# Kernel tuning notes

Hardware: AMD Instinct MI355X
Metric: run time of the kernel (lower is better)

The kernel has to match this reference:

```python
import jax, jax.numpy as jnp
import numpy as np

B, C, D, H, W = 4, 1, 192, 192, 192
SMALL = 4            # int(192 * bias_scale=0.025)
BIAS_STD = 0.7
MAX_SIGMA = 3.0
TRUNCATE = 4.0
K = 2 * int(TRUNCATE * MAX_SIGMA) + 1   # fixed truncated kernel size = 25
N_LABELS = 32
TABLE = 128          # static remap-table size (>= max source label, >= max dest)


def setup_inputs() -> dict:
    key = jax.random.key(0)
    k1, k2, k3, k4, k5 = jax.random.split(key, 5)
    return {
        "x": jax.random.normal(k1, (B, C, D, H, W), jnp.float32),
        "small_bias": jax.random.normal(k2, (B, 1, SMALL, SMALL, SMALL), jnp.float32),
        "sigma01": jax.random.uniform(k3, (B, 3), jnp.float32),
        "labels": jax.random.randint(k4, (B, 1, D, H, W), 0, N_LABELS, jnp.int32),
        "source_values": jnp.arange(N_LABELS, dtype=jnp.int64),
        "dest_values": jax.random.randint(k5, (N_LABELS,), 0, 100, jnp.int64),
    }


def _lin_weights(n_in, n_out):
    """Dense 1D linear-interp matrix [n_out, n_in], align_corners=True."""
    pos = jnp.linspace(0.0, n_in - 1.0, n_out)
    i0 = jnp.clip(jnp.floor(pos).astype(jnp.int32), 0, n_in - 2)
    f = pos - i0.astype(pos.dtype)
    r = jnp.arange(n_out)
    Wm = jnp.zeros((n_out, n_in), jnp.float32)
    Wm = Wm.at[r, i0].add(1.0 - f).at[r, i0 + 1].add(f)
    return Wm


def _bias_field(small_bias):
    # trilinear align_corners upsample [B,1,s,s,s] -> [B,1,D,H,W], separable
    b = small_bias * BIAS_STD
    b = jnp.einsum('bcxyz,dx->bcdyz', b, _lin_weights(SMALL, D))
    b = jnp.einsum('bcdyz,hy->bcdhz', b, _lin_weights(SMALL, H))
    b = jnp.einsum('bcdhz,wz->bcdhw', b, _lin_weights(SMALL, W))
    return b


def _gauss_kernels(sigma):
    """sigma [3] -> normalized kernels [3, K]; identity (delta) where sigma<0.01."""
    ar = jnp.arange(K, dtype=jnp.float32) - K // 2
    s = jnp.maximum(sigma, 1e-3)[:, None]
    g = jnp.exp(-0.5 * (ar[None, :] ** 2) / (s ** 2))
    g = g / g.sum(-1, keepdims=True)
    delta = jnp.zeros((K,), jnp.float32).at[K // 2].set(1.0)
    return jnp.where(sigma[:, None] >= 0.01, g, delta[None, :])


def _blur_axis(x, k, axis):
    # x [C,D,H,W]; depthwise 1D conv along `axis` with replicate (edge) padding
    p = K // 2
    xm = jnp.moveaxis(x, axis, -1)
    shp = xm.shape
    xm = xm.reshape(-1, 1, shp[-1])
    xm = jnp.pad(xm, ((0, 0), (0, 0), (p, p)), mode='edge')
    out = jax.lax.conv_general_dilated(xm, k.reshape(1, 1, K), (1,), 'VALID')
    return jnp.moveaxis(out.reshape(shp), -1, axis)


def _blur_sample(x, kernels):
    # x [C,D,H,W], kernels [3,K]; separable blur over D,H,W
    for i, ax in enumerate((1, 2, 3)):
        x = _blur_axis(x, kernels[i], ax)
    return x


def reference(x, small_bias, sigma01, labels, source_values, dest_values):
    # 1) bias-field corruption: x * exp(upsampled random field)
    img = x * jnp.exp(_bias_field(small_bias))
    # 2) dynamic per-sample Gaussian blur, sigma in [0, MAX_SIGMA]
    kernels = jax.vmap(_gauss_kernels)(sigma01 * MAX_SIGMA)   # [B,3,K]
    img = jax.vmap(_blur_sample)(img, kernels)
    # 3) label remap via lookup table gather
    mapping = jnp.zeros((TABLE,), jnp.int32).at[source_values].set(
        dest_values.astype(jnp.int32))
    labels_out = mapping[labels]
    return img, labels_out
```

## Files before the change

### kernel.cpp

```cpp
#include <hip/hip_runtime.h>
#include <hip/hip_fp16.h>
#include <cstdint>
#include <cstddef>

#define Bc 4
#define Dd 192
#define Hh 192
#define Ww 192
#define KK 25
#define RR 12
#define VOL (Bc*Dd*Hh*Ww)
#define SP 216
#define SPU (SP/2)
#define SH 98
#define RIN 56
#define RD  56

typedef unsigned short u16;
typedef unsigned int   u32;
typedef __fp16 h2 __attribute__((ext_vector_type(2)));
typedef __fp16 h8 __attribute__((ext_vector_type(8)));
typedef float  f32x4 __attribute__((ext_vector_type(4)));

__device__ inline u32 pk2(float a, float b) {
    return __builtin_bit_cast(u32, __builtin_amdgcn_cvt_pkrtz(a, b));
}

__global__ void setup_tables_kernel(const float* __restrict__ sigma01,
                                    const int* __restrict__ src,
                                    const int* __restrict__ dst,
                                    u32* __restrict__ kern2,
                                    int* __restrict__ mapping,
                                    float* __restrict__ mapf) {
    int t = threadIdx.x;
    if (t < 128) mapping[t] = 0;
    __syncthreads();
    if (t < 32) {
        int s = src[t];
        if (s >= 0 && s < 128) mapping[s] = dst[t];
    }
    __syncthreads();
    if (t < 128) mapf[t] = (float)mapping[t];
    if (t < Bc * 3) {
        float sig = sigma01[t] * 3.0f;
        float s = fmaxf(sig, 1e-3f);
        float g[KK];
        float sum = 0.0f;
        #pragma unroll
        for (int i = 0; i < KK; i++) {
            float a = (float)(i - RR);
            float v = expf(-0.5f * a * a / (s * s));
            g[i] = v; sum += v;
        }
        float inv = 1.0f / sum;
        #pragma unroll
        for (int i = 0; i < KK; i++) {
            float v = g[i] * inv;
            if (sig < 0.01f) v = (i == RR) ? 1.0f : 0.0f;
            u16 hb = __builtin_bit_cast(u16, __float2half(v));
            kern2[t * KK + i] = (u32)hb | ((u32)hb << 16);
        }
    }
}

__global__ __launch_bounds__(256) void pass_wh_remap_kernel(
    const float* __restrict__ x, u16* __restrict__ outB,
    const u32* __restrict__ kern2, const float* __restrict__ sb,
    const int4* __restrict__ labels, float4* __restrict__ lab_out,
    const float* __restrict__ mapf) {
    __shared__ u16 P[RIN * SP];
    __shared__ float2 ch2[RIN * 3];
    __shared__ u16 kpadW[64];
    const int tid = threadIdx.x;
    const int hx = blockIdx.x;
    const int d  = blockIdx.y;
    const int b  = blockIdx.z;

    if (tid < RIN) {
        int r = tid;
        int hrow = min(max(32 * hx - RR + r, 0), Hh - 1);
        float pos_d = d * (3.0f / 191.0f);
        int   id0   = min((int)pos_d, 2);
        float fd    = pos_d - (float)id0;
        float pos_h = hrow * (3.0f / 191.0f);
        int   ih0   = min((int)pos_h, 2);
        float fh    = pos_h - (float)ih0;
        const float* sbA = sb + b * 64 + id0 * 16 + ih0 * 4;
        float c[4];
        #pragma unroll
        for (int k = 0; k < 4; k++) {
            float v00 = sbA[k],      v01 = sbA[4 + k];
            float v10 = sbA[16 + k], v11 = sbA[20 + k];
            float vd0 = (1.f - fd) * v00 + fd * v10;
            float vd1 = (1.f - fd) * v01 + fd * v11;
            c[k] = ((1.f - fh) * vd0 + fh * vd1) * 0.7f;
        }
        #pragma unroll
        for (int k = 0; k < 3; k++)
            ch2[r * 3 + k] = make_float2(c[k], c[k + 1] - c[k]);
    }
    if (tid >= 64 && tid < 128) {
        int i = tid - 64;
        int t = i - 15;
        u16 v = (t >= 0 && t < KK) ? (u16)(kern2[(b * 3 + 2) * KK + t] & 0xFFFFu)
                                   : (u16)0;
        kpadW[i] = v;
    }
    __syncthreads();

    const size_t pbase = ((size_t)b * Dd + d) * (size_t)(Hh * Ww);
    #pragma unroll
    for (int it = 0; it < 11; it++) {
        int i4 = it * 256 + tid;
        if (i4 < RIN * 48) {
            int r = i4 / 48, w4 = i4 % 48;
            int w = 4 * w4;
            int hrow = min(max(32 * hx - RR + r, 0), Hh - 1);
            float4 v = *(const float4*)(x + pbase + (size_t)hrow * Ww + w);
            float rs[4];
            #pragma unroll
            for (int j = 0; j < 4; j++) {
                float pw = (float)(w + j) * (3.0f / 191.0f);
                int sel = (pw >= 1.0f) + (pw >= 2.0f);
                float2 cd = ch2[r * 3 + sel];
                float bias = fmaf(pw - (float)sel, cd.y, cd.x);
                float val = (j == 0 ? v.x : j == 1 ? v.y : j == 2 ? v.z : v.w);
                rs[j] = val * __expf(bias);
            }
            u32* dstp = (u32*)&P[r * SP + RR + w];
            dstp[0] = pk2(rs[0], rs[1]);
            dstp[1] = pk2(rs[2], rs[3]);
            if (w4 == 0) {
                u32 hh = pk2(rs[0], rs[0]);
                u32* hp = (u32*)&P[r * SP];
                #pragma unroll
                for (int m = 0; m < 6; m++) hp[m] = hh;
            } else if (w4 == 47) {
                u32 hh = pk2(rs[3], rs[3]);
                u32* hp = (u32*)&P[r * SP + RR + Ww];
                #pragma unroll
                for (int m = 0; m < 6; m++) hp[m] = hh;
            }
        }
    }
    __syncthreads();

    {
        const int bid = (b * Dd + d) * 6 + hx;
        const int4* lp = labels + (size_t)bid * 1536 + tid;
        int4 lab[6];
        #pragma unroll
        for (int m = 0; m < 6; m++) lab[m] = lp[m * 256];
        float4* op = lab_out + (size_t)bid * 1536 + tid;
        #pragma unroll
        for (int m = 0; m < 6; m++) {
            int4 l = lab[m];
            float4 o;
            o.x = mapf[min(max(l.x, 0), 127)];
            o.y = mapf[min(max(l.y, 0), 127)];
            o.z = mapf[min(max(l.z, 0), 127)];
            o.w = mapf[min(max(l.w, 0), 127)];
            op[m * 256] = o;
        }
    }

    {
        const int ln = tid & 63, wv = tid >> 6;
        const int c  = ln & 15;
        const int kg = ln >> 4;
        h8 B0, B1;
        #pragma unroll
        for (int j = 0; j < 8; j++) {
            int k = kg * 8 + j;
            B0[j] = __builtin_bit_cast(__fp16, kpadW[15 + k - c]);
            int i1 = 15 + k + 32 - c;
            B1[j] = __builtin_bit_cast(__fp16, (i1 < 64) ? kpadW[i1] : (u16)0);
        }
        const int ra = min(wv * 16 + c, RIN - 1);
        const u16* rowp = &P[ra * SP + kg * 8];
        const int rd0 = wv * 16 + kg * 4;
        h8 F[10];
        #pragma unroll
        for (int f = 0; f < 10; f++)
            F[f] = __builtin_bit_cast(h8, *(const uint4*)(rowp + f * 16));
        #pragma unroll
        for (int ct = 0; ct < 8; ct++) {
            f32x4 acc = {0.f, 0.f, 0.f, 0.f};
            acc = __builtin_amdgcn_mfma_f32_16x16x32_f16(F[ct], B0, acc, 0, 0, 0);
            acc = __builtin_amdgcn_mfma_f32_16x16x32_f16(F[ct + 2], B1, acc, 0, 0, 0);
            #pragma unroll
            for (int m = 0; m < 4; m++) {
                int rd = rd0 + m;
                if (rd < RIN)
                    P[rd * SP + RR + ct * 16 + c] =
                        __builtin_bit_cast(u16, (__fp16)acc[m]);
            }
        }
        h8 G[4];
        G[0] = __builtin_bit_cast(h8, *(const uint4*)(rowp + 160));
        G[1] = __builtin_bit_cast(h8, *(const uint4*)(rowp + 176));
        G[2] = __builtin_bit_cast(h8, *(const uint4*)(rowp + ((kg == 0) ? 192 : 160)));
        G[3] = __builtin_bit_cast(h8, *(const uint4*)(rowp + ((kg == 0) ? 208 : 160)));
        #pragma unroll
        for (int ct = 8; ct < 12; ct++) {
            h8 A0 = (ct < 10) ? F[ct] : G[ct - 10];
            h8 A1 = G[ct - 8];
            f32x4 acc = {0.f, 0.f, 0.f, 0.f};
            acc = __builtin_amdgcn_mfma_f32_16x16x32_f16(A0, B0, acc, 0, 0, 0);
            acc = __builtin_amdgcn_mfma_f32_16x16x32_f16(A1, B1, acc, 0, 0, 0);
            #pragma unroll
            for (int m = 0; m < 4; m++) {
                int rd = rd0 + m;
                if (rd < RIN)
                    P[rd * SP + RR + ct * 16 + c] =
                        __builtin_bit_cast(u16, (__fp16)acc[m]);
            }
        }
    }
    __syncthreads();

    {
        const u32* kh2 = kern2 + (b * 3 + 1) * KK;
        u32* outp = (u32*)(outB + pbase);
        #pragma unroll
        for (int it = 0; it < 2; it++) {
            int item = it * 256 + tid;
            if (item < 384) {
                int col = item % 96;
                int g = item / 96;
                u32 win[32];
                #pragma unroll
                for (int i = 0; i < 32; i++)
                    win[i] = *((const u32*)P + (g * 8 + i) * SPU + 6 + col);
                h2 acc[8];
                #pragma unroll
                for (int j = 0; j < 8; j++) acc[j] = (h2)(0.0f);
                #pragma unroll
                for (int t = 0; t < KK; t++) {
                    h2 kv = __builtin_bit_cast(h2, kh2[t]);
                    #pragma unroll
                    for (int j = 0; j < 8; j++)
                        acc[j] += kv * __builtin_bit_cast(h2, win[j + t]);
                }
                #pragma unroll
                for (int j = 0; j < 8; j++)
                    outp[(32 * hx + g * 8 + j) * 96 + col] =
                        __builtin_bit_cast(u32, acc[j]);
            }
        }
    }
}

__global__ __launch_bounds__(192) void pass_d_kernel(
    const u16* __restrict__ in, float* __restrict__ img,
    const u32* __restrict__ kern2) {
    __shared__ __attribute__((aligned(16))) u16 T[RD * SH];
    const int tid = threadIdx.x;
    const int w0 = blockIdx.x * 96;
    const int d0 = blockIdx.y * 32;
    const int z = blockIdx.z;
    const int h = z % Hh, b = z / Hh;
    const u32* kp = kern2 + b * 3 * KK;
    #pragma unroll
    for (int k = 0; k < 4; k++) {
        int idx = k * 192 + tid;
        if (idx < RD * 12) {
            int r = idx / 12, sg = idx % 12;
            int dd = min(max(d0 + r - RR, 0), Dd - 1);
            uint4 v = *(const uint4*)(in + (((size_t)b * Dd + dd) * Hh + h) * (size_t)Ww + w0 + sg * 8);
            u32* p = (u32*)&T[r * SH + sg * 8];
            p[0] = v.x; p[1] = v.y; p[2] = v.z; p[3] = v.w;
        }
    }
    __syncthreads();
    const int p = tid % 48;
    const int g = tid / 48;
    const int ob = g * 8;
    u32 win[32];
    #pragma unroll
    for (int i = 0; i < 32; i++) win[i] = *(const u32*)&T[(ob + i) * SH + 2 * p];
    h2 acc[8];
    #pragma unroll
    for (int j = 0; j < 8; j++) acc[j] = (h2)(0.0f);
    #pragma unroll
    for (int t = 0; t < KK; t++) {
        h2 kv = __builtin_bit_cast(h2, kp[t]);
        #pragma unroll
        for (int j = 0; j < 8; j++)
            acc[j] += kv * __builtin_bit_cast(h2, win[j + t]);
    }
    #pragma unroll
    for (int j = 0; j < 8; j++) {
        h2 a = acc[j];
        float2 f = make_float2((float)a.x, (float)a.y);
        *(float2*)(img + (((size_t)b * Dd + (d0 + ob + j)) * Hh + h) * (size_t)Ww + w0 + 2 * p) = f;
    }
}

extern "C" void kernel_launch(void* const* d_in, const int* in_sizes, int n_in,
                              void* d_out, int out_size, void* d_ws, size_t ws_size,
                              hipStream_t stream) {
    const float* x          = (const float*)d_in[0];
    const float* small_bias = (const float*)d_in[1];
    const float* sigma01    = (const float*)d_in[2];
    const int*   labels     = (const int*)d_in[3];
    const int*   src        = (const int*)d_in[4];
    const int*   dst        = (const int*)d_in[5];

    float* out     = (float*)d_out;
    float* img     = out;
    float* lab_out = out + (size_t)VOL;

    u32*   kern2   = (u32*)((float*)d_ws + 384);
    int*   mapping = (int*)((float*)d_ws + 768);
    float* mapf    = (float*)d_ws + 896;
    u16*   Bb      = (u16*)((char*)d_ws + 8192);

    setup_tables_kernel<<<1, 128, 0, stream>>>(sigma01, src, dst, kern2,
                                               mapping, mapf);

    pass_wh_remap_kernel<<<dim3(6, Dd, Bc), 256, 0, stream>>>(
        x, Bb, kern2, small_bias,
        (const int4*)labels, (float4*)lab_out, mapf);
    pass_d_kernel<<<dim3(Ww / 96, Dd / 32, Bc * Hh), 192, 0, stream>>>(Bb, img, kern2);
}
```

Baseline: 134.3 us.

## Fold setup kernel into blur kernels by computing taps and remap table per block

Drops the separate setup_tables launch. Each block now computes its own Gaussian taps in-kernel with fast exp, and the W/H kernel builds the label remap table in shared memory. The point is to remove one kernel launch and its serialization, and to keep blur taps in registers instead of reading them from global memory. The W/H load loop is also changed so each thread handles a fixed column with its interpolation coefficients precomputed, using 240 active threads over 12 iterations. The cost is redundant tap math in every block, slightly different exp precision, and some idle threads in the load loop.

```diff
diff --git a/kernel.cpp b/kernel.cpp
--- a/kernel.cpp
+++ b/kernel.cpp
@@ -26,51 +26,32 @@
     return __builtin_bit_cast(u32, __builtin_amdgcn_cvt_pkrtz(a, b));
 }
 
-__global__ void setup_tables_kernel(const float* __restrict__ sigma01,
-                                    const int* __restrict__ src,
-                                    const int* __restrict__ dst,
-                                    u32* __restrict__ kern2,
-                                    int* __restrict__ mapping,
-                                    float* __restrict__ mapf) {
-    int t = threadIdx.x;
-    if (t < 128) mapping[t] = 0;
-    __syncthreads();
-    if (t < 32) {
-        int s = src[t];
-        if (s >= 0 && s < 128) mapping[s] = dst[t];
-    }
-    __syncthreads();
-    if (t < 128) mapf[t] = (float)mapping[t];
-    if (t < Bc * 3) {
-        float sig = sigma01[t] * 3.0f;
-        float s = fmaxf(sig, 1e-3f);
-        float g[KK];
-        float sum = 0.0f;
-        #pragma unroll
-        for (int i = 0; i < KK; i++) {
-            float a = (float)(i - RR);
-            float v = expf(-0.5f * a * a / (s * s));
-            g[i] = v; sum += v;
-        }
-        float inv = 1.0f / sum;
-        #pragma unroll
-        for (int i = 0; i < KK; i++) {
-            float v = g[i] * inv;
-            if (sig < 0.01f) v = (i == RR) ? 1.0f : 0.0f;
-            u16 hb = __builtin_bit_cast(u16, __float2half(v));
-            kern2[t * KK + i] = (u32)hb | ((u32)hb << 16);
-        }
-    }
+__device__ inline float gauss_tap(float s01, int idx) {
+    float sig = s01 * 3.0f;
+    float s = fmaxf(sig, 1e-3f);
+    float inv2 = -0.5f / (s * s);
+    float sum = 0.0f;
+    #pragma unroll
+    for (int i = 0; i < KK; i++) {
+        float a = (float)(i - RR);
+        sum += __expf(a * a * inv2);
+    }
+    float a = (float)(idx - RR);
+    float v = __expf(a * a * inv2) / sum;
+    if (sig < 0.01f) v = (idx == RR) ? 1.0f : 0.0f;
+    return v;
 }
 
 __global__ __launch_bounds__(256) void pass_wh_remap_kernel(
     const float* __restrict__ x, u16* __restrict__ outB,
-    const u32* __restrict__ kern2, const float* __restrict__ sb,
-    const int4* __restrict__ labels, float4* __restrict__ lab_out,
-    const float* __restrict__ mapf) {
+    const float* __restrict__ sigma01, const float* __restrict__ sb,
+    const int* __restrict__ src, const int* __restrict__ dst,
+    const int4* __restrict__ labels, float4* __restrict__ lab_out) {
     __shared__ u16 P[RIN * SP];
     __shared__ float2 ch2[RIN * 3];
     __shared__ u16 kpadW[64];
+    __shared__ u32 khp[25];
+    __shared__ float Lmap[128];
     const int tid = threadIdx.x;
     const int hx = blockIdx.x;
     const int d  = blockIdx.y;
@@ -99,47 +80,70 @@
         for (int k = 0; k < 3; k++)
             ch2[r * 3 + k] = make_float2(c[k], c[k + 1] - c[k]);
     }
-    if (tid >= 64 && tid < 128) {
-        int i = tid - 64;
-        int t = i - 15;
-        u16 v = (t >= 0 && t < KK) ? (u16)(kern2[(b * 3 + 2) * KK + t] & 0xFFFFu)
-                                   : (u16)0;
+    if (tid >= 56 && tid < 184) Lmap[tid - 56] = 0.0f;
+    if (tid >= 56 && tid < 81) {
+        int i = tid - 56;
+        float v = gauss_tap(sigma01[b * 3 + 1], i);
+        u16 hb = __builtin_bit_cast(u16, __float2half(v));
+        khp[i] = (u32)hb | ((u32)hb << 16);
+    }
+    if (tid >= 184 && tid < 248) {
+        int i = tid - 184;
+        int tt = i - 15;
+        u16 v = 0;
+        if (tt >= 0 && tt < KK)
+            v = __builtin_bit_cast(u16, __float2half(gauss_tap(sigma01[b * 3 + 2], tt)));
         kpadW[i] = v;
     }
     __syncthreads();
 
+    if (tid < 32) {
+        int s = src[tid];
+        if (s >= 0 && s < 128) Lmap[s] = (float)dst[tid];
+    }
+
     const size_t pbase = ((size_t)b * Dd + d) * (size_t)(Hh * Ww);
-    #pragma unroll
-    for (int it = 0; it < 11; it++) {
-        int i4 = it * 256 + tid;
-        if (i4 < RIN * 48) {
-            int r = i4 / 48, w4 = i4 % 48;
-            int w = 4 * w4;
-            int hrow = min(max(32 * hx - RR + r, 0), Hh - 1);
-            float4 v = *(const float4*)(x + pbase + (size_t)hrow * Ww + w);
-            float rs[4];
-            #pragma unroll
-            for (int j = 0; j < 4; j++) {
-                float pw = (float)(w + j) * (3.0f / 191.0f);
-                int sel = (pw >= 1.0f) + (pw >= 2.0f);
-                float2 cd = ch2[r * 3 + sel];
-                float bias = fmaf(pw - (float)sel, cd.y, cd.x);
-                float val = (j == 0 ? v.x : j == 1 ? v.y : j == 2 ? v.z : v.w);
-                rs[j] = val * __expf(bias);
-            }
-            u32* dstp = (u32*)&P[r * SP + RR + w];
-            dstp[0] = pk2(rs[0], rs[1]);
-            dstp[1] = pk2(rs[2], rs[3]);
-            if (w4 == 0) {
-                u32 hh = pk2(rs[0], rs[0]);
-                u32* hp = (u32*)&P[r * SP];
-                #pragma unroll
-                for (int m = 0; m < 6; m++) hp[m] = hh;
-            } else if (w4 == 47) {
-                u32 hh = pk2(rs[3], rs[3]);
-                u32* hp = (u32*)&P[r * SP + RR + Ww];
-                #pragma unroll
-                for (int m = 0; m < 6; m++) hp[m] = hh;
+    {
+        const int w4 = tid % 48;
+        const int rloc = tid / 48;
+        const int w = 4 * w4;
+        float fwj[4];
+        int   selj[4];
+        #pragma unroll
+        for (int j = 0; j < 4; j++) {
+            float pw = (float)(w + j) * (3.0f / 191.0f);
+            int sel = (pw >= 1.0f) + (pw >= 2.0f);
+            selj[j] = sel;
+            fwj[j] = pw - (float)sel;
+        }
+        #pragma unroll
+        for (int it = 0; it < 12; it++) {
+            int row = it * 5 + rloc;
+            if (tid < 240 && row < RIN) {
+                int hrow = min(max(32 * hx - RR + row, 0), Hh - 1);
+                float4 v = *(const float4*)(x + pbase + (size_t)hrow * Ww + w);
+                float rs[4];
+                #pragma unroll
+                for (int j = 0; j < 4; j++) {
+                    float2 cd = ch2[row * 3 + selj[j]];
+                    float bias = fmaf(fwj[j], cd.y, cd.x);
+                    float val = (j == 0 ? v.x : j == 1 ? v.y : j == 2 ? v.z : v.w);
+                    rs[j] = val * __expf(bias);
+                }
+                u32* dstp = (u32*)&P[row * SP + RR + w];
+                dstp[0] = pk2(rs[0], rs[1]);
+                dstp[1] = pk2(rs[2], rs[3]);
+                if (w4 == 0) {
+                    u32 hh = pk2(rs[0], rs[0]);
+                    u32* hp = (u32*)&P[row * SP];
+                    #pragma unroll
+                    for (int m = 0; m < 6; m++) hp[m] = hh;
+                } else if (w4 == 47) {
+                    u32 hh = pk2(rs[3], rs[3]);
+                    u32* hp = (u32*)&P[row * SP + RR + Ww];
+                    #pragma unroll
+                    for (int m = 0; m < 6; m++) hp[m] = hh;
+                }
             }
         }
     }
@@ -156,10 +160,10 @@
         for (int m = 0; m < 6; m++) {
             int4 l = lab[m];
             float4 o;
-            o.x = mapf[min(max(l.x, 0), 127)];
-            o.y = mapf[min(max(l.y, 0), 127)];
-            o.z = mapf[min(max(l.z, 0), 127)];
-            o.w = mapf[min(max(l.w, 0), 127)];
+            o.x = Lmap[min(max(l.x, 0), 127)];
+            o.y = Lmap[min(max(l.y, 0), 127)];
+            o.z = Lmap[min(max(l.z, 0), 127)];
+            o.w = Lmap[min(max(l.w, 0), 127)];
             op[m * 256] = o;
         }
     }
@@ -220,7 +224,9 @@
     __syncthreads();
 
     {
-        const u32* kh2 = kern2 + (b * 3 + 1) * KK;
+        u32 khr[KK];
+        #pragma unroll
+        for (int t = 0; t < KK; t++) khr[t] = khp[t];
         u32* outp = (u32*)(outB + pbase);
         #pragma unroll
         for (int it = 0; it < 2; it++) {
@@ -237,7 +243,7 @@
                 for (int j = 0; j < 8; j++) acc[j] = (h2)(0.0f);
                 #pragma unroll
                 for (int t = 0; t < KK; t++) {
-                    h2 kv = __builtin_bit_cast(h2, kh2[t]);
+                    h2 kv = __builtin_bit_cast(h2, khr[t]);
                     #pragma unroll
                     for (int j = 0; j < 8; j++)
                         acc[j] += kv * __builtin_bit_cast(h2, win[j + t]);
@@ -253,14 +259,19 @@
 
 __global__ __launch_bounds__(192) void pass_d_kernel(
     const u16* __restrict__ in, float* __restrict__ img,
-    const u32* __restrict__ kern2) {
+    const float* __restrict__ sigma01) {
     __shared__ __attribute__((aligned(16))) u16 T[RD * SH];
+    __shared__ u32 kdp[25];
     const int tid = threadIdx.x;
     const int w0 = blockIdx.x * 96;
     const int d0 = blockIdx.y * 32;
     const int z = blockIdx.z;
     const int h = z % Hh, b = z / Hh;
-    const u32* kp = kern2 + b * 3 * KK;
+    if (tid < 25) {
+        float v = gauss_tap(sigma01[b * 3 + 0], tid);
+        u16 hb = __builtin_bit_cast(u16, __float2half(v));
+        kdp[tid] = (u32)hb | ((u32)hb << 16);
+    }
     #pragma unroll
     for (int k = 0; k < 4; k++) {
         int idx = k * 192 + tid;
@@ -273,6 +284,9 @@
         }
     }
     __syncthreads();
+    u32 kdr[KK];
+    #pragma unroll
+    for (int t = 0; t < KK; t++) kdr[t] = kdp[t];
     const int p = tid % 48;
     const int g = tid / 48;
     const int ob = g * 8;
@@ -284,7 +298,7 @@
     for (int j = 0; j < 8; j++) acc[j] = (h2)(0.0f);
     #pragma unroll
     for (int t = 0; t < KK; t++) {
-        h2 kv = __builtin_bit_cast(h2, kp[t]);
+        h2 kv = __builtin_bit_cast(h2, kdr[t]);
         #pragma unroll
         for (int j = 0; j < 8; j++)
             acc[j] += kv * __builtin_bit_cast(h2, win[j + t]);
@@ -310,17 +324,11 @@
     float* out     = (float*)d_out;
     float* img     = out;
     float* lab_out = out + (size_t)VOL;
-
-    u32*   kern2   = (u32*)((float*)d_ws + 384);
-    int*   mapping = (int*)((float*)d_ws + 768);
-    float* mapf    = (float*)d_ws + 896;
     u16*   Bb      = (u16*)((char*)d_ws + 8192);
 
-    setup_tables_kernel<<<1, 128, 0, stream>>>(sigma01, src, dst, kern2,
-                                               mapping, mapf);
-
     pass_wh_remap_kernel<<<dim3(6, Dd, Bc), 256, 0, stream>>>(
-        x, Bb, kern2, small_bias,
-        (const int4*)labels, (float4*)lab_out, mapf);
-    pass_d_kernel<<<dim3(Ww / 96, Dd / 32, Bc * Hh), 192, 0, stream>>>(Bb, img, kern2);
-}
+        x, Bb, sigma01, small_bias, src, dst,
+        (const int4*)labels, (float4*)lab_out);
+    pass_d_kernel<<<dim3(Ww / 96, Dd / 32, Bc * Hh), 192, 0, stream>>>(
+        Bb, img, sigma01);
+}
```

New measurement: 128.3 us. -4.4%, faster.
